# Kernel tuning notes

Measured on AMD Instinct MI355X. Metric: run time of the kernel, lower is better.

The kernel has to match this reference:

```python
import jax, jax.numpy as jnp
import numpy as np

N = 50000      # nodes
E = 800000     # edges (before self loops)
IN = 128       # in_channels
H = 4          # heads
C = 32         # hidden_channels (per head)
D = H * C      # concat output dim = 128
NEG_SLOPE = 0.2
LN_EPS = 1e-5


def setup_inputs() -> dict:
    key = jax.random.key(0)
    ks = jax.random.split(key, 24)
    def p(k, shape, s=0.1):
        return jax.random.normal(k, shape, dtype=jnp.float32) * s
    inp = {
        "x": p(ks[0], (N, IN), 1.0),
        "edge_index": jax.random.randint(ks[1], (2, E), 0, N, dtype=jnp.int32),
    }
    i = 2
    for l, ind in [(0, IN), (1, D)]:
        inp[f"Wl{l}"] = p(ks[i], (ind, D)); i += 1
        inp[f"bl{l}"] = p(ks[i], (D,), 0.02); i += 1
        inp[f"Wr{l}"] = p(ks[i], (ind, D)); i += 1
        inp[f"br{l}"] = p(ks[i], (D,), 0.02); i += 1
        inp[f"att{l}"] = p(ks[i], (H, C)); i += 1
        inp[f"Wres{l}"] = p(ks[i], (ind, D)); i += 1
        inp[f"bias{l}"] = p(ks[i], (D,), 0.02); i += 1
        inp[f"g{l}"] = jnp.ones((D,), jnp.float32)
        inp[f"be{l}"] = jnp.zeros((D,), jnp.float32)
    return inp


def _gatv2_layer(x, src, dst, Wl, bl, Wr, br, att, Wres, bias):
    """GATv2Conv with concat heads, add_self_loops already applied, residual."""
    n = x.shape[0]
    xl = (x @ Wl + bl).reshape(n, H, C)   # source transform
    xr = (x @ Wr + br).reshape(n, H, C)   # target transform
    # edge-level attention logits: e = a . LeakyReLU(xl[j] + xr[i])  [E, H]
    eh = jax.nn.leaky_relu(xl[src] + xr[dst], negative_slope=NEG_SLOPE)  # [E,H,C]
    score = jnp.einsum('ehc,hc->eh', eh, att)                            # [E,H]
    # segment softmax over incoming edges of each destination node
    smax = jax.ops.segment_max(score, dst, num_segments=n)               # [N,H]
    ex = jnp.exp(score - smax[dst])
    ssum = jax.ops.segment_sum(ex, dst, num_segments=n)                  # [N,H]
    alpha = ex / ssum[dst]                                               # [E,H]
    msg = xl[src] * alpha[:, :, None]                                    # [E,H,C]
    out = jax.ops.segment_sum(msg, dst, num_segments=n).reshape(n, D)
    return out + x @ Wres + bias  # residual (bias=False linear) + final bias


def _layernorm_relu(x, g, b):
    mu = jnp.mean(x, axis=-1, keepdims=True)
    var = jnp.mean(jnp.square(x - mu), axis=-1, keepdims=True)
    return jax.nn.relu((x - mu) * jax.lax.rsqrt(var + LN_EPS) * g + b)


def reference(x, edge_index,
              Wl0, bl0, Wr0, br0, att0, Wres0, bias0, g0, be0,
              Wl1, bl1, Wr1, br1, att1, Wres1, bias1, g1, be1):
    n = x.shape[0]
    loops = jnp.arange(n, dtype=edge_index.dtype)
    src = jnp.concatenate([edge_index[0], loops])  # add_self_loops=True
    dst = jnp.concatenate([edge_index[1], loops])
    h = _gatv2_layer(x, src, dst, Wl0, bl0, Wr0, br0, att0, Wres0, bias0)
    h = _layernorm_relu(h, g0, be0)
    h = _gatv2_layer(h, src, dst, Wl1, bl1, Wr1, br1, att1, Wres1, bias1)
    h = _layernorm_relu(h, g1, be1)
    return h
```

## Files before the change

kernel.cpp:

```cpp
#include <hip/hip_runtime.h>
#include <math.h>

#define D 128
#define LRELU 0.2f
#define LN_EPS 1e-5f
#define INV_LN2 1.4426950408889634f

#define NBMAX 512
#define CAP 4096
#define P1CHUNK 8192

typedef __attribute__((ext_vector_type(8))) short short8;
typedef __attribute__((ext_vector_type(8))) unsigned short ushort8;
typedef __attribute__((ext_vector_type(4))) float f32x4;
typedef __attribute__((ext_vector_type(2))) float f32x2;
typedef __attribute__((ext_vector_type(2))) unsigned int u32x2;

static __device__ __forceinline__ unsigned short f2bf(float f) {
    union { float f; unsigned u; } a; a.f = f;
    unsigned r = a.u + 0x7FFFu + ((a.u >> 16) & 1u);
    return (unsigned short)(r >> 16);
}

static __device__ __forceinline__ f32x2 pk_add(f32x2 a, f32x2 b) {
    f32x2 d; asm("v_pk_add_f32 %0, %1, %2" : "=v"(d) : "v"(a), "v"(b)); return d;
}
static __device__ __forceinline__ f32x2 pk_mul(f32x2 a, f32x2 b) {
    f32x2 d; asm("v_pk_mul_f32 %0, %1, %2" : "=v"(d) : "v"(a), "v"(b)); return d;
}
static __device__ __forceinline__ f32x2 pk_fma(f32x2 a, f32x2 b, f32x2 c) {
    f32x2 d; asm("v_pk_fma_f32 %0, %1, %2, %3" : "=v"(d) : "v"(a), "v"(b), "v"(c)); return d;
}
static __device__ __forceinline__ f32x2 pk_abs(f32x2 a) {
    u32x2 u = __builtin_bit_cast(u32x2, a);
    u &= 0x7FFFFFFFu;
    return __builtin_bit_cast(f32x2, u);
}
static __device__ __forceinline__ f32x2 bf2x(unsigned u) {
    f32x2 r;
    r.x = __uint_as_float(u << 16);
    r.y = __uint_as_float(u & 0xFFFF0000u);
    return r;
}

static __device__ __forceinline__ float red4_dpp(float p) {
    int v = __builtin_amdgcn_update_dpp(0, __builtin_bit_cast(int, p), 0xB1, 0xf, 0xf, true);
    p += __builtin_bit_cast(float, v);
    v = __builtin_amdgcn_update_dpp(0, __builtin_bit_cast(int, p), 0x4E, 0xf, 0xf, true);
    p += __builtin_bit_cast(float, v);
    return p;
}


__global__ __launch_bounds__(256) void k_prep(
    const int* __restrict__ srcp, const int* __restrict__ dstp,
    int* __restrict__ bcur, unsigned* __restrict__ ebuf, int E, int N,
    const float* __restrict__ X, ushort* __restrict__ Xb, int Mp,
    const float* __restrict__ W0, const float* __restrict__ W1, const float* __restrict__ W2,
    const float* __restrict__ W3, const float* __restrict__ W4, const float* __restrict__ W5,
    ushort* __restrict__ Wp, int nP1, int nCV)
{
    const int bx = blockIdx.x;
    const int tid = threadIdx.x;
    if (bx < nP1) {
        __shared__ int h[NBMAX];
        const int E2 = E + N;
        const int e0 = bx * P1CHUNK;
        const int e1 = min(e0 + P1CHUNK, E2);
        for (int t = tid; t < NBMAX; t += 256) h[t] = 0;
        __syncthreads();
        for (int e = e0 + tid; e < e1; e += 256) {
            int d = (e < E) ? dstp[e] : e - E;
            atomicAdd(&h[d >> 7], 1);
        }
        __syncthreads();
        for (int b = tid; b < NBMAX; b += 256) {
            int c = h[b];
            h[b] = c ? atomicAdd(&bcur[b], c) : 0;
        }
        __syncthreads();
        for (int e = e0 + tid; e < e1; e += 256) {
            int d  = (e < E) ? dstp[e] : e - E;
            int sc = (e < E) ? srcp[e] : e - E;
            int b = d >> 7;
            int pos = atomicAdd(&h[b], 1) & (CAP - 1);
            ebuf[(size_t)b * CAP + pos] = ((unsigned)sc << 7) | (unsigned)(d & 127);
        }
    } else if (bx < nP1 + nCV) {
        int idx = (bx - nP1) * 256 + tid;
        if (idx >= Mp * (D / 4)) return;
        ushort4 o;
        if (idx < N * (D / 4)) {
            float4 v = ((const float4*)X)[idx];
            o.x = f2bf(v.x); o.y = f2bf(v.y); o.z = f2bf(v.z); o.w = f2bf(v.w);
        } else {
            o = make_ushort4(0, 0, 0, 0);
        }
        ((ushort4*)Xb)[idx] = o;
    } else {
        int bid = bx - nP1 - nCV;
        int m = bid >> 6;
        int o = ((bid & 63) << 8) + tid;
        const float* W;
        if (m == 0) W = W0; else if (m == 1) W = W1; else if (m == 2) W = W2;
        else if (m == 3) W = W3; else if (m == 4) W = W4; else W = W5;
        int j  = o & 7;
        int l  = (o >> 3) & 63;
        int ct = (o >> 9) & 7;
        int kc = o >> 12;
        int k   = kc * 32 + ((l >> 4) << 3) + j;
        int col = (ct << 4) + (l & 15);
        Wp[m * 16384 + o] = f2bf(W[k * D + col]);
    }
}


__global__ __launch_bounds__(256) void bhist_kernel(const unsigned* __restrict__ ebuf,
                                                    const int* __restrict__ bcur,
                                                    int* __restrict__ deg,
                                                    int* __restrict__ btot, int N) {
    const int b = blockIdx.x;
    const int base = b << 7;
    const int tid = threadIdx.x;
    __shared__ int h[128];
    __shared__ int t2[2];
    if (tid < 128) h[tid] = 0;
    __syncthreads();
    const int cnt = min(bcur[b], CAP);
    for (int k = tid; k < cnt; k += 256) {
        unsigned v = ebuf[(size_t)b * CAP + k];
        atomicAdd(&h[v & 127], 1);
    }
    __syncthreads();
    int v = (tid < 128) ? h[tid] : 0;
    if (tid < 128 && base + tid < N) deg[base + tid] = v;
    #pragma unroll
    for (int o = 32; o >= 1; o >>= 1) v += __shfl_xor(v, o);
    if (tid == 0)  t2[0] = v;
    if (tid == 64) t2[1] = v;
    __syncthreads();
    if (tid == 0) btot[b] = t2[0] + t2[1];
}


static __device__ __forceinline__ void gemm_body(
    int bxg, int seg, int tid,
    const ushort* __restrict__ Xb, const ushort* __restrict__ Wp,
    const float* __restrict__ bl, const float* __restrict__ br,
    ushort* __restrict__ XLb, ushort* __restrict__ XRb, float* __restrict__ RES)
{
    const int l = tid & 63;
    const int wave = tid >> 6;
    const int wr = wave >> 1, wc = wave & 1;
    const int brow = bxg * 128 + wr * 64;
    const ushort* W = Wp + seg * 16384;

    f32x4 acc[4][4] = {};
    const int arow = brow + (l & 15);
    const int koff = (l >> 4) * 8;

    #pragma unroll
    for (int kc = 0; kc < 4; ++kc) {
        short8 A[4], B[4];
        #pragma unroll
        for (int at = 0; at < 4; ++at)
            A[at] = *(const short8*)&Xb[(size_t)(arow + at * 16) * D + kc * 32 + koff];
        #pragma unroll
        for (int ct = 0; ct < 4; ++ct) {
            int ctg = wc * 4 + ct;
            B[ct] = *(const short8*)&W[(((kc * 8 + ctg) * 64) + l) * 8];
        }
        #pragma unroll
        for (int at = 0; at < 4; ++at)
            #pragma unroll
            for (int ct = 0; ct < 4; ++ct)
                acc[at][ct] = __builtin_amdgcn_mfma_f32_16x16x32_bf16(A[at], B[ct], acc[at][ct], 0, 0, 0);
    }

    const int c = l & 15;
    const int r0 = (l >> 4) * 4;
    const float* bias = (seg == 0) ? bl : ((seg == 1) ? br : nullptr);
    #pragma unroll
    for (int ct = 0; ct < 4; ++ct) {
        int gcol = wc * 64 + ct * 16 + c;
        float bv = bias ? bias[gcol] : 0.f;
        #pragma unroll
        for (int at = 0; at < 4; ++at) {
            #pragma unroll
            for (int r = 0; r < 4; ++r) {
                int grow = brow + at * 16 + r0 + r;
                float v = acc[at][ct][r] + bv;
                size_t off = (size_t)grow * D + gcol;
                if (seg == 0)      XLb[off] = f2bf(v);
                else if (seg == 1) XRb[off] = f2bf(v);
                else               RES[off] = v;
            }
        }
    }
}


__global__ __launch_bounds__(256) void k_mid(
    const unsigned* __restrict__ ebuf, const int* __restrict__ bcur,
    const int* __restrict__ deg, const int* __restrict__ btot,
    int* __restrict__ off, int* __restrict__ csrc, int N, int NB, int nblk,
    const ushort* __restrict__ Xb, const ushort* __restrict__ Wp,
    const float* __restrict__ bl, const float* __restrict__ br,
    ushort* __restrict__ XLb, ushort* __restrict__ XRb, float* __restrict__ RES)
{
    const int bx = blockIdx.x;
    if (bx < NB) {
        const int b = bx;
        const int base = b << 7;
        const int tid = threadIdx.x;
        __shared__ int cur[128];
        __shared__ int wsum[4];
        __shared__ int wtot[2];

        int acc = 0;
        for (int t = tid; t < b; t += 256) acc += btot[t];
        #pragma unroll
        for (int o = 32; o >= 1; o >>= 1) acc += __shfl_xor(acc, o);
        if ((tid & 63) == 0) wsum[tid >> 6] = acc;
        __syncthreads();
        const int B = wsum[0] + wsum[1] + wsum[2] + wsum[3];

        int dv = 0;
        if (tid < 128 && base + tid < N) dv = deg[base + tid];
        int incl = dv;
        if (tid < 128) {
            #pragma unroll
            for (int o = 1; o < 64; o <<= 1) {
                int u = __shfl_up(incl, o);
                if ((tid & 63) >= o) incl += u;
            }
        }
        if (tid == 63)  wtot[0] = incl;
        if (tid == 127) wtot[1] = incl;
        __syncthreads();
        if (tid < 128) {
            int add = (tid >= 64) ? wtot[0] : 0;
            int excl = B + add + incl - dv;
            cur[tid] = excl;
            if (base + tid < N) off[base + tid] = excl;
        }
        if (b == NB - 1 && tid == 0) off[N] = B + wtot[0] + wtot[1];
        __syncthreads();

        const int cnt = min(bcur[b], CAP);
        for (int k = tid; k < cnt; k += 256) {
            unsigned v = ebuf[(size_t)b * CAP + k];
            int p = atomicAdd(&cur[v & 127], 1);
            csrc[p] = v >> 7;
        }
    } else {
        int bid = bx - NB;
        int seg = bid / nblk;
        int bxg = bid - seg * nblk;
        gemm_body(bxg, seg, threadIdx.x, Xb, Wp, bl, br, XLb, XRb, RES);
    }
}

__global__ __launch_bounds__(256) void gemm_mfma(
    const ushort* __restrict__ Xb, const ushort* __restrict__ Wp,
    const float* __restrict__ bl, const float* __restrict__ br,
    ushort* __restrict__ XLb, ushort* __restrict__ XRb, float* __restrict__ RES)
{
    gemm_body(blockIdx.x, blockIdx.y, threadIdx.x, Xb, Wp, bl, br, XLb, XRb, RES);
}


__global__ __launch_bounds__(256) void gat_node(
    const ushort* __restrict__ XLb, const ushort* __restrict__ XRb, const float* __restrict__ RES,
    const float* __restrict__ att, const float* __restrict__ bias,
    const float* __restrict__ g, const float* __restrict__ be,
    const int* __restrict__ off, const int* __restrict__ csrc,
    float* __restrict__ OUTf, ushort* __restrict__ OUTb)
{
    const int l = threadIdx.x & 63;
    const int i = blockIdx.x * 16 + (threadIdx.x >> 6) * 4 + (l >> 4);
    const int f = (l & 15) * 8;
    const unsigned ibase = ((unsigned)i << 7) + f;
    const int lb = l & 48;

    f32x2 at06[4], at04[4];
    #pragma unroll
    for (int k = 0; k < 4; ++k) {
        float2 a = *(const float2*)&att[f + k * 2];
        f32x2 av; av.x = a.x; av.y = a.y;
        at06[k] = av * (0.6f * INV_LN2);
        at04[k] = av * (0.4f * INV_LN2);
    }

    uint4 xru = *(const uint4*)&XRb[ibase];
    f32x2 xr2[4];
    xr2[0] = bf2x(xru.x); xr2[1] = bf2x(xru.y); xr2[2] = bf2x(xru.z); xr2[3] = bf2x(xru.w);

    const int e0 = off[i], e1 = off[i + 1];
    const int len = e1 - e0;
    int mx = max(len, __shfl_xor(len, 16));
    mx = max(mx, __shfl_xor(mx, 32));

    float m = -1e30f, s = 0.f;
    f32x2 a2[4] = {};

    for (int c0 = 0; c0 < mx; c0 += 16) {
        int myj = csrc[min(e0 + c0 + (l & 15), e1 - 1)];
        const int rem = mx - c0;
        const int nbb = min(4, (rem + 3) >> 2);
        const int kleft = len - c0;

        uint4 u_[4];
        {
            int s0 = __shfl(myj, lb + 0);
            int s1 = __shfl(myj, lb + 1);
            int s2 = __shfl(myj, lb + 2);
            int s3 = __shfl(myj, lb + 3);
            u_[0] = *(const uint4*)&XLb[((unsigned)s0 << 7) + f];
            u_[1] = *(const uint4*)&XLb[((unsigned)s1 << 7) + f];
            u_[2] = *(const uint4*)&XLb[((unsigned)s2 << 7) + f];
            u_[3] = *(const uint4*)&XLb[((unsigned)s3 << 7) + f];
        }

        #pragma unroll
        for (int bb = 0; bb < 4; ++bb) {
            if (bb >= nbb) break;
            uint4 uc[4];
            #pragma unroll
            for (int j = 0; j < 4; ++j) uc[j] = u_[j];
            if (bb + 1 < nbb) {
                int s0 = __shfl(myj, lb + (bb + 1) * 4 + 0);
                int s1 = __shfl(myj, lb + (bb + 1) * 4 + 1);
                int s2 = __shfl(myj, lb + (bb + 1) * 4 + 2);
                int s3 = __shfl(myj, lb + (bb + 1) * 4 + 3);
                u_[0] = *(const uint4*)&XLb[((unsigned)s0 << 7) + f];
                u_[1] = *(const uint4*)&XLb[((unsigned)s1 << 7) + f];
                u_[2] = *(const uint4*)&XLb[((unsigned)s2 << 7) + f];
                u_[3] = *(const uint4*)&XLb[((unsigned)s3 << 7) + f];
            }

            const int kb = kleft - bb * 4;
            f32x2 xp[4][4];
            float p[4];
            #pragma unroll
            for (int j = 0; j < 4; ++j) {
                xp[j][0] = bf2x(uc[j].x);
                xp[j][1] = bf2x(uc[j].y);
                xp[j][2] = bf2x(uc[j].z);
                xp[j][3] = bf2x(uc[j].w);
                f32x2 v0 = pk_add(xp[j][0], xr2[0]);
                f32x2 pj2 = pk_mul(v0, at06[0]);
                pj2 = pk_fma(pk_abs(v0), at04[0], pj2);
                #pragma unroll
                for (int k = 1; k < 4; ++k) {
                    f32x2 v = pk_add(xp[j][k], xr2[k]);
                    pj2 = pk_fma(v, at06[k], pj2);
                    pj2 = pk_fma(pk_abs(v), at04[k], pj2);
                }
                float pj = pj2.x + pj2.y;
                pj = red4_dpp(pj);
                p[j] = (j < kb) ? pj : -1e30f;
            }
            float pmax = fmaxf(fmaxf(p[0], p[1]), fmaxf(p[2], p[3]));
            float nm = fmaxf(m, pmax);
            float so = exp2f(m - nm);
            float w0 = exp2f(p[0] - nm), w1 = exp2f(p[1] - nm);
            float w2 = exp2f(p[2] - nm), w3 = exp2f(p[3] - nm);
            s = s * so + ((w0 + w1) + (w2 + w3));
            f32x2 so2; so2.x = so; so2.y = so;
            f32x2 w02; w02.x = w0; w02.y = w0;
            f32x2 w12; w12.x = w1; w12.y = w1;
            f32x2 w22; w22.x = w2; w22.y = w2;
            f32x2 w32; w32.x = w3; w32.y = w3;
            #pragma unroll
            for (int k = 0; k < 4; ++k) {
                f32x2 t = pk_mul(xp[0][k], w02);
                t = pk_fma(xp[1][k], w12, t);
                t = pk_fma(xp[2][k], w22, t);
                t = pk_fma(xp[3][k], w32, t);
                a2[k] = pk_fma(a2[k], so2, t);
            }
            m = nm;
        }
    }

    const float4 rsA = *(const float4*)&RES[ibase];
    const float4 rsB = *(const float4*)&RES[ibase + 4];
    const float4 biA = *(const float4*)&bias[f];
    const float4 biB = *(const float4*)&bias[f + 4];
    float inv = 1.f / s;
    float r0 = a2[0].x * inv + rsA.x + biA.x;
    float r1 = a2[0].y * inv + rsA.y + biA.y;
    float r2 = a2[1].x * inv + rsA.z + biA.z;
    float r3 = a2[1].y * inv + rsA.w + biA.w;
    float r4 = a2[2].x * inv + rsB.x + biB.x;
    float r5 = a2[2].y * inv + rsB.y + biB.y;
    float r6 = a2[3].x * inv + rsB.z + biB.z;
    float r7 = a2[3].y * inv + rsB.w + biB.w;

    float sum = ((r0 + r1) + (r2 + r3)) + ((r4 + r5) + (r6 + r7));
    float sq  = ((r0 * r0 + r1 * r1) + (r2 * r2 + r3 * r3))
              + ((r4 * r4 + r5 * r5) + (r6 * r6 + r7 * r7));
    #pragma unroll
    for (int o = 8; o >= 1; o >>= 1) {
        sum += __shfl_xor(sum, o);
        sq  += __shfl_xor(sq, o);
    }
    float mu  = sum * (1.f / 128.f);
    float var = sq * (1.f / 128.f) - mu * mu;
    float isd = rsqrtf(var + LN_EPS);
    const float4 gvA = *(const float4*)&g[f];
    const float4 gvB = *(const float4*)&g[f + 4];
    const float4 bvA = *(const float4*)&be[f];
    const float4 bvB = *(const float4*)&be[f + 4];
    float o0 = fmaxf((r0 - mu) * isd * gvA.x + bvA.x, 0.f);
    float o1 = fmaxf((r1 - mu) * isd * gvA.y + bvA.y, 0.f);
    float o2 = fmaxf((r2 - mu) * isd * gvA.z + bvA.z, 0.f);
    float o3 = fmaxf((r3 - mu) * isd * gvA.w + bvA.w, 0.f);
    float o4 = fmaxf((r4 - mu) * isd * gvB.x + bvB.x, 0.f);
    float o5 = fmaxf((r5 - mu) * isd * gvB.y + bvB.y, 0.f);
    float o6 = fmaxf((r6 - mu) * isd * gvB.z + bvB.z, 0.f);
    float o7 = fmaxf((r7 - mu) * isd * gvB.w + bvB.w, 0.f);

    if (OUTb) {
        ushort8 ob;
        ob[0] = f2bf(o0); ob[1] = f2bf(o1); ob[2] = f2bf(o2); ob[3] = f2bf(o3);
        ob[4] = f2bf(o4); ob[5] = f2bf(o5); ob[6] = f2bf(o6); ob[7] = f2bf(o7);
        *(ushort8*)&OUTb[ibase] = ob;
    } else {
        *(float4*)&OUTf[ibase]     = make_float4(o0, o1, o2, o3);
        *(float4*)&OUTf[ibase + 4] = make_float4(o4, o5, o6, o7);
    }
}


extern "C" void kernel_launch(void* const* d_in, const int* in_sizes, int n_in,
                              void* d_out, int out_size, void* d_ws, size_t ws_size,
                              hipStream_t stream)
{
    const float* x    = (const float*)d_in[0];
    const int*   ei   = (const int*)d_in[1];
    const float* Wl0  = (const float*)d_in[2];
    const float* bl0  = (const float*)d_in[3];
    const float* Wr0  = (const float*)d_in[4];
    const float* br0  = (const float*)d_in[5];
    const float* att0 = (const float*)d_in[6];
    const float* Wres0= (const float*)d_in[7];
    const float* bias0= (const float*)d_in[8];
    const float* g0   = (const float*)d_in[9];
    const float* be0  = (const float*)d_in[10];
    const float* Wl1  = (const float*)d_in[11];
    const float* bl1  = (const float*)d_in[12];
    const float* Wr1  = (const float*)d_in[13];
    const float* br1  = (const float*)d_in[14];
    const float* att1 = (const float*)d_in[15];
    const float* Wres1= (const float*)d_in[16];
    const float* bias1= (const float*)d_in[17];
    const float* g1   = (const float*)d_in[18];
    const float* be1  = (const float*)d_in[19];

    const int N  = in_sizes[0] / D;
    const int E  = in_sizes[1] / 2;
    const int E2 = E + N;
    const int nblk = (N + 127) / 128;
    const int Mp = nblk * 128;
    const int NB = nblk;

    char* w = (char*)d_ws;
    ushort* Xb  = (ushort*)w; w += (size_t)Mp * D * 2;
    ushort* Hb  = (ushort*)w; w += (size_t)Mp * D * 2;
    ushort* XLb = (ushort*)w; w += (size_t)Mp * D * 2;
    ushort* XRb = (ushort*)w; w += (size_t)Mp * D * 2;
    float*  RES = (float*)w;  w += (size_t)Mp * D * 4;
    ushort* Wp  = (ushort*)w; w += (size_t)6 * 16384 * 2;
    int* deg     = (int*)w; w += (size_t)N * 4;
    int* off     = (int*)w; w += (size_t)(N + 1) * 4;
    int* bcur    = (int*)w; w += (size_t)NBMAX * 4;
    int* btot    = (int*)w; w += (size_t)NBMAX * 4;
    unsigned* ebuf = (unsigned*)w; w += (size_t)NB * CAP * 4;
    int* csrc    = (int*)w; w += (size_t)E2 * 4;

    const int* srcp = ei;
    const int* dstp = ei + E;

    const int nP1 = (E2 + P1CHUNK - 1) / P1CHUNK;
    const int nCV = (Mp * (D / 4) + 255) / 256;
    const int nPW = 6 * 64;
    const int nGM = nblk * 3;

    hipMemsetAsync(bcur, 0, (size_t)NBMAX * 4, stream);
    k_prep<<<nP1 + nCV + nPW, 256, 0, stream>>>(srcp, dstp, bcur, ebuf, E, N,
                                                x, Xb, Mp,
                                                Wl0, Wr0, Wres0, Wl1, Wr1, Wres1,
                                                Wp, nP1, nCV);
    bhist_kernel<<<NB, 256, 0, stream>>>(ebuf, bcur, deg, btot, N);

    k_mid<<<NB + nGM, 256, 0, stream>>>(ebuf, bcur, deg, btot, off, csrc, N, NB, nblk,
                                        Xb, Wp, bl0, br0, XLb, XRb, RES);

    const int gatg = N / 16;
    dim3 ggrid(nblk, 3);

    gat_node<<<gatg, 256, 0, stream>>>(XLb, XRb, RES, att0, bias0, g0, be0, off, csrc, nullptr, Hb);
    gemm_mfma<<<ggrid, 256, 0, stream>>>(Hb, Wp + 3 * 16384, bl1, br1, XLb, XRb, RES);
    gat_node<<<gatg, 256, 0, stream>>>(XLb, XRb, RES, att1, bias1, g1, be1, off, csrc, (float*)d_out, nullptr);
}
```

Before: 183.1 us.

## Fuse degree histogram into k_mid and degree-sort nodes for gat_node balance

Removes the separate bhist kernel by computing each bucket's per-node degree histogram inside k_mid and using bcur directly as the bucket edge total for the prefix sum. It also counting-sorts the nodes of each 128-node bucket by degree into an ord array, and gat_node reads its node index through ord. Grouping nodes of similar degree into the same wavefront is meant to reduce divergence in edge-loop trip counts. The cost is an extra indirection, less contiguous node access, and a second pass over ebuf inside k_mid.

```diff
diff --git a/kernel.cpp b/kernel.cpp
--- a/kernel.cpp
+++ b/kernel.cpp
@@ -115,34 +115,6 @@
 }
 
 
-__global__ __launch_bounds__(256) void bhist_kernel(const unsigned* __restrict__ ebuf,
-                                                    const int* __restrict__ bcur,
-                                                    int* __restrict__ deg,
-                                                    int* __restrict__ btot, int N) {
-    const int b = blockIdx.x;
-    const int base = b << 7;
-    const int tid = threadIdx.x;
-    __shared__ int h[128];
-    __shared__ int t2[2];
-    if (tid < 128) h[tid] = 0;
-    __syncthreads();
-    const int cnt = min(bcur[b], CAP);
-    for (int k = tid; k < cnt; k += 256) {
-        unsigned v = ebuf[(size_t)b * CAP + k];
-        atomicAdd(&h[v & 127], 1);
-    }
-    __syncthreads();
-    int v = (tid < 128) ? h[tid] : 0;
-    if (tid < 128 && base + tid < N) deg[base + tid] = v;
-    #pragma unroll
-    for (int o = 32; o >= 1; o >>= 1) v += __shfl_xor(v, o);
-    if (tid == 0)  t2[0] = v;
-    if (tid == 64) t2[1] = v;
-    __syncthreads();
-    if (tid == 0) btot[b] = t2[0] + t2[1];
-}
-
-
 static __device__ __forceinline__ void gemm_body(
     int bxg, int seg, int tid,
     const ushort* __restrict__ Xb, const ushort* __restrict__ Wp,
@@ -202,8 +174,8 @@
 
 __global__ __launch_bounds__(256) void k_mid(
     const unsigned* __restrict__ ebuf, const int* __restrict__ bcur,
-    const int* __restrict__ deg, const int* __restrict__ btot,
-    int* __restrict__ off, int* __restrict__ csrc, int N, int NB, int nblk,
+    int* __restrict__ off, int* __restrict__ ord, int* __restrict__ csrc,
+    int N, int NB, int nblk,
     const ushort* __restrict__ Xb, const ushort* __restrict__ Wp,
     const float* __restrict__ bl, const float* __restrict__ br,
     ushort* __restrict__ XLb, ushort* __restrict__ XRb, float* __restrict__ RES)
@@ -213,20 +185,32 @@
         const int b = bx;
         const int base = b << 7;
         const int tid = threadIdx.x;
+        const int cntN = min(128, N - base);
+        __shared__ int h[128];
         __shared__ int cur[128];
+        __shared__ int d2h[64];
+        __shared__ int sord[128];
         __shared__ int wsum[4];
         __shared__ int wtot[2];
 
         int acc = 0;
-        for (int t = tid; t < b; t += 256) acc += btot[t];
+        for (int t = tid; t < b; t += 256) acc += bcur[t];
         #pragma unroll
         for (int o = 32; o >= 1; o >>= 1) acc += __shfl_xor(acc, o);
         if ((tid & 63) == 0) wsum[tid >> 6] = acc;
+        if (tid < 128) h[tid] = 0;
+        if (tid < 64) d2h[tid] = 0;
         __syncthreads();
         const int B = wsum[0] + wsum[1] + wsum[2] + wsum[3];
 
-        int dv = 0;
-        if (tid < 128 && base + tid < N) dv = deg[base + tid];
+        const int cnt = min(bcur[b], CAP);
+        for (int k = tid; k < cnt; k += 256) {
+            unsigned v = ebuf[(size_t)b * CAP + k];
+            atomicAdd(&h[v & 127], 1);
+        }
+        __syncthreads();
+
+        int dv = (tid < 128) ? h[tid] : 0;
         int incl = dv;
         if (tid < 128) {
             #pragma unroll
@@ -242,12 +226,30 @@
             int add = (tid >= 64) ? wtot[0] : 0;
             int excl = B + add + incl - dv;
             cur[tid] = excl;
-            if (base + tid < N) off[base + tid] = excl;
+            if (tid < cntN) off[base + tid] = excl;
         }
         if (b == NB - 1 && tid == 0) off[N] = B + wtot[0] + wtot[1];
-        __syncthreads();
-
-        const int cnt = min(bcur[b], CAP);
+
+        if (tid < cntN) atomicAdd(&d2h[min(dv, 63)], 1);
+        __syncthreads();
+        if (tid < 64) {
+            int v2 = d2h[tid];
+            int inc2 = v2;
+            #pragma unroll
+            for (int o = 1; o < 64; o <<= 1) {
+                int u = __shfl_up(inc2, o);
+                if (tid >= o) inc2 += u;
+            }
+            d2h[tid] = inc2 - v2;
+        }
+        __syncthreads();
+        if (tid < cntN) {
+            int pos = atomicAdd(&d2h[min(dv, 63)], 1);
+            sord[pos] = tid;
+        }
+        __syncthreads();
+        if (tid < cntN) ord[base + tid] = base + sord[tid];
+
         for (int k = tid; k < cnt; k += 256) {
             unsigned v = ebuf[(size_t)b * CAP + k];
             int p = atomicAdd(&cur[v & 127], 1);
@@ -274,11 +276,12 @@
     const ushort* __restrict__ XLb, const ushort* __restrict__ XRb, const float* __restrict__ RES,
     const float* __restrict__ att, const float* __restrict__ bias,
     const float* __restrict__ g, const float* __restrict__ be,
-    const int* __restrict__ off, const int* __restrict__ csrc,
+    const int* __restrict__ off, const int* __restrict__ csrc, const int* __restrict__ ord,
     float* __restrict__ OUTf, ushort* __restrict__ OUTb)
 {
     const int l = threadIdx.x & 63;
-    const int i = blockIdx.x * 16 + (threadIdx.x >> 6) * 4 + (l >> 4);
+    const int slot = blockIdx.x * 16 + (threadIdx.x >> 6) * 4 + (l >> 4);
+    const int i = ord[slot];
     const int f = (l & 15) * 8;
     const unsigned ibase = ((unsigned)i << 7) + f;
     const int lb = l & 48;
@@ -473,10 +476,9 @@
     ushort* XRb = (ushort*)w; w += (size_t)Mp * D * 2;
     float*  RES = (float*)w;  w += (size_t)Mp * D * 4;
     ushort* Wp  = (ushort*)w; w += (size_t)6 * 16384 * 2;
-    int* deg     = (int*)w; w += (size_t)N * 4;
     int* off     = (int*)w; w += (size_t)(N + 1) * 4;
+    int* ord     = (int*)w; w += (size_t)N * 4;
     int* bcur    = (int*)w; w += (size_t)NBMAX * 4;
-    int* btot    = (int*)w; w += (size_t)NBMAX * 4;
     unsigned* ebuf = (unsigned*)w; w += (size_t)NB * CAP * 4;
     int* csrc    = (int*)w; w += (size_t)E2 * 4;
 
@@ -493,15 +495,14 @@
                                                 x, Xb, Mp,
                                                 Wl0, Wr0, Wres0, Wl1, Wr1, Wres1,
                                                 Wp, nP1, nCV);
-    bhist_kernel<<<NB, 256, 0, stream>>>(ebuf, bcur, deg, btot, N);
-
-    k_mid<<<NB + nGM, 256, 0, stream>>>(ebuf, bcur, deg, btot, off, csrc, N, NB, nblk,
+
+    k_mid<<<NB + nGM, 256, 0, stream>>>(ebuf, bcur, off, ord, csrc, N, NB, nblk,
                                         Xb, Wp, bl0, br0, XLb, XRb, RES);
 
     const int gatg = N / 16;
     dim3 ggrid(nblk, 3);
 
-    gat_node<<<gatg, 256, 0, stream>>>(XLb, XRb, RES, att0, bias0, g0, be0, off, csrc, nullptr, Hb);
+    gat_node<<<gatg, 256, 0, stream>>>(XLb, XRb, RES, att0, bias0, g0, be0, off, csrc, ord, nullptr, Hb);
     gemm_mfma<<<ggrid, 256, 0, stream>>>(Hb, Wp + 3 * 16384, bl1, br1, XLb, XRb, RES);
-    gat_node<<<gatg, 256, 0, stream>>>(XLb, XRb, RES, att1, bias1, g1, be1, off, csrc, (float*)d_out, nullptr);
-}
+    gat_node<<<gatg, 256, 0, stream>>>(XLb, XRb, RES, att1, bias1, g1, be1, off, csrc, ord, (float*)d_out, nullptr);
+}
```

New measurement: 191.8 us. +4.8%, slower.
